# Kernel tuning notes

Hardware: AMD Instinct MI355X
Metric: run time of the kernel (lower is better)

The kernel has to match this reference:

```python
import jax, jax.numpy as jnp
import numpy as np

HALF_LOG_2PI = 0.9189385332046727  # 0.5*log(2*pi)


def _sum_layer(prod, logits):
    # prod: [B, R, KK] child log-probs; logits: [R, KK, K] unnormalized sum weights
    W = jax.nn.softmax(logits, axis=1)            # normalized mixture weights
    m = jnp.max(prod, axis=-1, keepdims=True)     # stable logsumexp via einsum
    e = jnp.exp(prod - m)                         # [B, R, KK]
    s = jnp.einsum('brc,rck->brk', e, W)          # [B, R, K]
    return jnp.log(s) + m


def setup_inputs() -> dict:
    key = jax.random.key(0)
    ks = jax.random.split(key, 12)
    B, F, K = 8192, 256, 8
    inp = {
        'x': jax.random.normal(ks[0], (B, F), dtype=jnp.float32),
        'mu': jax.random.normal(ks[1], (F, K), dtype=jnp.float32),
        'log_sigma': jax.random.uniform(ks[2], (F, K), dtype=jnp.float32),
    }
    R = F // 2
    for i in range(8):
        inp['w%d' % i] = jax.random.normal(ks[3 + i], (R, K * K, K), dtype=jnp.float32)
        R //= 2
    inp['root_w'] = jax.random.normal(ks[11], (K,), dtype=jnp.float32)
    return inp


def reference(x, mu, log_sigma, w0, w1, w2, w3, w4, w5, w6, w7, root_w):
    # Gaussian leaf log-probs: [B, F, K]
    z = (x[:, :, None] - mu) * jnp.exp(-log_sigma)
    h = -0.5 * z * z - log_sigma - HALF_LOG_2PI
    # Alternating product (pair adjacent regions) / sum (mix KK -> K) layers
    for w in (w0, w1, w2, w3, w4, w5, w6, w7):
        B, R, K = h.shape
        prod = (h[:, 0::2, :, None] + h[:, 1::2, None, :]).reshape(B, R // 2, K * K)
        h = _sum_layer(prod, w)
    # Root sum node over the K dists of the single remaining region -> [B]
    lp = h[:, 0, :] + jax.nn.log_softmax(root_w)
    return jax.scipy.special.logsumexp(lp, axis=-1)
```

## Files before the change

kernel.cpp:

```cpp
#include <hip/hip_runtime.h>
#include <math.h>

#define NTH 256

static constexpr float HLP = 0.9189385332046727f;

typedef __attribute__((ext_vector_type(2))) _Float16 half2v;
typedef __attribute__((ext_vector_type(2))) __fp16   fp16x2;

static constexpr int L3MF = 524288;
static constexpr size_t WS_NEED_B = (size_t)655360 * 4;

__device__ __forceinline__ half2v pkrtz(float a, float b) {
  return __builtin_bit_cast(half2v, __builtin_amdgcn_cvt_pkrtz(a, b));
}
__device__ __forceinline__ half2v u2h(unsigned u) {
  return __builtin_bit_cast(half2v, u);
}
__device__ __forceinline__ unsigned h2u(half2v h) {
  return __builtin_bit_cast(unsigned, h);
}
__device__ __forceinline__ float dd(half2v a, half2v b, float c) {
#if __has_builtin(__builtin_amdgcn_fdot2)
  return __builtin_amdgcn_fdot2(__builtin_bit_cast(fp16x2, a),
                                __builtin_bit_cast(fp16x2, b), c, false);
#else
  return fmaf((float)a[0], (float)b[0], fmaf((float)a[1], (float)b[1], c));
#endif
}
__device__ __forceinline__ float max8(const float* s) {
  float m = s[0];
  #pragma unroll
  for (int k = 1; k < 8; ++k) m = fmaxf(m, s[k]);
  return m;
}

__device__ __forceinline__ void leaf_ii(float xv, const float* mu8, const float* A8,
                                        const float* B8, half2v* ii, float* M) {
  float h[8];
  float m = -3.0e38f;
  #pragma unroll
  for (int k = 0; k < 8; ++k) {
    const float z = (xv - mu8[k]) * A8[k];
    h[k] = fmaf(-0.5f * z, z, B8[k]);
    m = fmaxf(m, h[k]);
  }
  #pragma unroll
  for (int k = 0; k < 8; ++k) {
    const float n = __expf(h[k] - m);
    ii[k] = pkrtz(n, n);
  }
  *M = m;
}
__device__ __forceinline__ void leaf_pk(float xv, const float* mu8, const float* A8,
                                        const float* B8, half2v* pk, float* M) {
  float h[8];
  float m = -3.0e38f;
  #pragma unroll
  for (int k = 0; k < 8; ++k) {
    const float z = (xv - mu8[k]) * A8[k];
    h[k] = fmaf(-0.5f * z, z, B8[k]);
    m = fmaxf(m, h[k]);
  }
  #pragma unroll
  for (int p = 0; p < 4; ++p) {
    const float n0 = __expf(h[2 * p] - m);
    const float n1 = __expf(h[2 * p + 1] - m);
    pk[p] = pkrtz(n0, n1);
  }
  *M = m;
}

template<int G, bool OUT_II>
__device__ __forceinline__ void combine_d2(const uint4* __restrict__ WL,
                                           const half2v (&na)[G][8],
                                           const half2v (&nb)[G][4],
                                           half2v (&oii)[G][8],
                                           half2v (&opk)[G][4],
                                           float (&M)[G]) {
  float s[G][8];
  #pragma unroll
  for (int g = 0; g < G; ++g)
    #pragma unroll
    for (int k = 0; k < 8; ++k) s[g][k] = 0.f;

  #pragma unroll
  for (int i = 0; i < 8; ++i) {
    half2v e[G][4];
    #pragma unroll
    for (int g = 0; g < G; ++g) {
      e[g][0] = na[g][i] * nb[g][0];
      e[g][1] = na[g][i] * nb[g][1];
      e[g][2] = na[g][i] * nb[g][2];
      e[g][3] = na[g][i] * nb[g][3];
    }
    #pragma unroll
    for (int k = 0; k < 8; ++k) {
      const uint4 w = WL[i * 8 + k];
      #pragma unroll
      for (int g = 0; g < G; ++g) {
        float acc = s[g][k];
        acc = dd(e[g][0], u2h(w.x), acc);
        acc = dd(e[g][1], u2h(w.y), acc);
        acc = dd(e[g][2], u2h(w.z), acc);
        acc = dd(e[g][3], u2h(w.w), acc);
        s[g][k] = acc;
      }
    }
  }
  #pragma unroll
  for (int g = 0; g < G; ++g) {
    const float smax = max8(s[g]);
    const float inv = 1.0f / smax;
    if constexpr (OUT_II) {
      #pragma unroll
      for (int p = 0; p < 8; ++p) {
        const float n = s[g][p] * inv;
        oii[g][p] = pkrtz(n, n);
      }
    } else {
      #pragma unroll
      for (int p = 0; p < 4; ++p)
        opk[g][p] = pkrtz(s[g][2 * p] * inv, s[g][2 * p + 1] * inv);
    }
    M[g] += __logf(smax);
  }
}

__device__ __forceinline__ void prep_col_std(const float* stage, unsigned* wdwL,
                                             int r, int k) {
  float v[64];
  float m = -3.0e38f;
  #pragma unroll
  for (int c = 0; c < 64; ++c) { v[c] = stage[r * 512 + c * 8 + k]; m = fmaxf(m, v[c]); }
  float t = 0.f;
  #pragma unroll
  for (int c = 0; c < 64; ++c) { v[c] = __expf(v[c] - m); t += v[c]; }
  const float inv = 1.0f / t;
  #pragma unroll
  for (int i = 0; i < 8; ++i)
    #pragma unroll
    for (int jp = 0; jp < 4; ++jp)
      wdwL[r * 256 + (i * 8 + k) * 4 + jp] =
          h2u(pkrtz(v[i * 8 + 2 * jp] * inv, v[i * 8 + 2 * jp + 1] * inv));
}

__device__ __forceinline__ void mk_ii(uint4 p, half2v* ii) {
  const half2v a0 = u2h(p.x), a1 = u2h(p.y), a2 = u2h(p.z), a3 = u2h(p.w);
  ii[0] = __builtin_shufflevector(a0, a0, 0, 0);
  ii[1] = __builtin_shufflevector(a0, a0, 1, 1);
  ii[2] = __builtin_shufflevector(a1, a1, 0, 0);
  ii[3] = __builtin_shufflevector(a1, a1, 1, 1);
  ii[4] = __builtin_shufflevector(a2, a2, 0, 0);
  ii[5] = __builtin_shufflevector(a2, a2, 1, 1);
  ii[6] = __builtin_shufflevector(a3, a3, 0, 0);
  ii[7] = __builtin_shufflevector(a3, a3, 1, 1);
}

template<bool OUT_II>
__device__ __forceinline__ void subtree_g2(
    const uint4* __restrict__ wA, const uint4* __restrict__ wB,
    const uint4* __restrict__ wT,
    const float* m0, const float* A0, const float* B0,
    float4 xa, float4 xb,
    half2v (&oii)[2][8], half2v (&opk)[2][4], float (&Mout)[2]) {
  half2v ii[2][8], pk[2][4];
  half2v aii[2][8], bpk[2][4];
  half2v dii[2][8], dpk[2][4];
  float Ma, Mb;

  leaf_ii(xa.x, m0,      A0,      B0,      ii[0], &Ma);
  leaf_pk(xa.y, m0 + 8,  A0 + 8,  B0 + 8,  pk[0], &Mb);
  float MA[2];
  MA[0] = Ma + Mb;
  leaf_ii(xb.x, m0,      A0,      B0,      ii[1], &Ma);
  leaf_pk(xb.y, m0 + 8,  A0 + 8,  B0 + 8,  pk[1], &Mb);
  MA[1] = Ma + Mb;
  combine_d2<2, true>(wA, ii, pk, aii, dpk, MA);

  leaf_ii(xa.z, m0 + 16, A0 + 16, B0 + 16, ii[0], &Ma);
  leaf_pk(xa.w, m0 + 24, A0 + 24, B0 + 24, pk[0], &Mb);
  float MB[2];
  MB[0] = Ma + Mb;
  leaf_ii(xb.z, m0 + 16, A0 + 16, B0 + 16, ii[1], &Ma);
  leaf_pk(xb.w, m0 + 24, A0 + 24, B0 + 24, pk[1], &Mb);
  MB[1] = Ma + Mb;
  combine_d2<2, false>(wB, ii, pk, dii, bpk, MB);

  float M[2] = {MA[0] + MB[0], MA[1] + MB[1]};
  combine_d2<2, OUT_II>(wT, aii, bpk, oii, opk, M);
  Mout[0] = M[0];
  Mout[1] = M[1];
}

__global__ __launch_bounds__(NTH, 2) void spn_f(
    const float* __restrict__ x,
    const float* __restrict__ mu,
    const float* __restrict__ ls,
    const float* __restrict__ w0, const float* __restrict__ w1,
    const float* __restrict__ w2, const float* __restrict__ w3,
    float* __restrict__ ws)
{
  __shared__ float stage[7680];
  __shared__ uint4 wsh4[960];
  __shared__ float lsh[384];
  const int tid = threadIdx.x;
  const int r3 = blockIdx.x >> 5;
  const int chunk = blockIdx.x & 31;

  #pragma unroll
  for (int i = 0; i < 30; ++i) {
    const int idx = tid + 256 * i;
    const int reg = idx >> 9, off = idx & 511;
    const float* src;
    if (reg < 8)       src = w0 + (8 * r3 + reg) * 512;
    else if (reg < 12) src = w1 + (4 * r3 + (reg - 8)) * 512;
    else if (reg < 14) src = w2 + (2 * r3 + (reg - 12)) * 512;
    else               src = w3 + r3 * 512;
    stage[idx] = src[off];
  }
  if (tid < 128) {
    const int base = r3 * 128;
    const float l = ls[base + tid];
    lsh[tid]       = mu[base + tid];
    lsh[128 + tid] = __expf(-l);
    lsh[256 + tid] = -l - HLP;
  }
  __syncthreads();

  if (tid < 120) prep_col_std(stage, reinterpret_cast<unsigned*>(wsh4), tid >> 3, tid & 7);
  __syncthreads();

  uint4* exN = reinterpret_cast<uint4*>(stage);
  float* exM = stage + 2048;

  const int h = tid >> 7;
  const int u = tid & 127;
  const int b0 = chunk * 256 + u;
  {
    const float* xa = x + (size_t)b0 * 256 + 16 * r3 + 8 * h;
    const float* xb = x + (size_t)(b0 + 128) * 256 + 16 * r3 + 8 * h;
    const float4 xa0 = *reinterpret_cast<const float4*>(xa);
    const float4 xa1 = *reinterpret_cast<const float4*>(xa + 4);
    const float4 xb0 = *reinterpret_cast<const float4*>(xb);
    const float4 xb1 = *reinterpret_cast<const float4*>(xb + 4);

    const float* m0 = lsh + h * 64;
    const float* A0 = lsh + 128 + h * 64;
    const float* B0 = lsh + 256 + h * 64;
    const uint4* wL0 = wsh4 + (4 * h) * 64;
    const uint4* wL1 = wsh4 + (8 + 2 * h) * 64;
    const uint4* wL2 = wsh4 + (12 + h) * 64;

    half2v q0ii[2][8], q1pk[2][4];
    half2v dii[2][8], dpk[2][4];
    float Mq0[2], Mq1[2];

    subtree_g2<true >(wL0,        wL0 + 64,  wL1,      m0,      A0,      B0,
                      xa0, xb0, q0ii, dpk, Mq0);
    subtree_g2<false>(wL0 + 128,  wL0 + 192, wL1 + 64, m0 + 32, A0 + 32, B0 + 32,
                      xa1, xb1, dii, q1pk, Mq1);

    float M[2] = {Mq0[0] + Mq1[0], Mq0[1] + Mq1[1]};
    half2v n[2][4];
    combine_d2<2, false>(wL2, q0ii, q1pk, dii, n, M);

    exN[h * 256 + u]       = uint4{h2u(n[0][0]), h2u(n[0][1]), h2u(n[0][2]), h2u(n[0][3])};
    exN[h * 256 + u + 128] = uint4{h2u(n[1][0]), h2u(n[1][1]), h2u(n[1][2]), h2u(n[1][3])};
    exM[h * 256 + u]       = M[0];
    exM[h * 256 + u + 128] = M[1];
  }
  __syncthreads();

  if (tid < 128) {
    const uint4 p0a = exN[tid], p0b = exN[tid + 128];
    const uint4 p1a = exN[256 + tid], p1b = exN[256 + tid + 128];
    float M[2];
    M[0] = exM[tid]       + exM[256 + tid];
    M[1] = exM[tid + 128] + exM[256 + tid + 128];

    half2v ii[2][8], pk[2][4];
    half2v dii[2][8];
    mk_ii(p0a, ii[0]);
    mk_ii(p0b, ii[1]);
    pk[0][0] = u2h(p1a.x); pk[0][1] = u2h(p1a.y); pk[0][2] = u2h(p1a.z); pk[0][3] = u2h(p1a.w);
    pk[1][0] = u2h(p1b.x); pk[1][1] = u2h(p1b.y); pk[1][2] = u2h(p1b.z); pk[1][3] = u2h(p1b.w);

    half2v n[2][4];
    combine_d2<2, false>(wsh4 + 14 * 64, ii, pk, dii, n, M);

    const int b = chunk * 256 + tid;
    uint4* outn = reinterpret_cast<uint4*>(ws);
    outn[r3 * 8192 + b]       = uint4{h2u(n[0][0]), h2u(n[0][1]), h2u(n[0][2]), h2u(n[0][3])};
    outn[r3 * 8192 + b + 128] = uint4{h2u(n[1][0]), h2u(n[1][1]), h2u(n[1][2]), h2u(n[1][3])};
    ws[L3MF + r3 * 8192 + b]       = M[0];
    ws[L3MF + r3 * 8192 + b + 128] = M[1];
  }
}

__device__ __forceinline__ float macTd(const uint4* __restrict__ Wr, int myk,
                                       const float* na, const half2v* nbpk) {
  float s = 0.f;
  #pragma unroll
  for (int i = 0; i < 8; ++i) {
    const uint4 w = Wr[myk * 8 + ((i ^ myk) & 7)];
    float T = dd(nbpk[0], u2h(w.x), 0.f);
    T = dd(nbpk[1], u2h(w.y), T);
    T = dd(nbpk[2], u2h(w.z), T);
    T = dd(nbpk[3], u2h(w.w), T);
    s = fmaf(na[i], T, s);
  }
  return s;
}

__global__ __launch_bounds__(NTH) void spn_c(
    const float* __restrict__ w4, const float* __restrict__ w5,
    const float* __restrict__ w6, const float* __restrict__ w7,
    const float* __restrict__ root_w,
    float* __restrict__ ws,
    float* __restrict__ out)
{
  __shared__ float stage[7680];
  __shared__ uint4 wsh4[960];
  __shared__ float ssh[8];
  const int tid = threadIdx.x;

  #pragma unroll
  for (int i = 0; i < 30; ++i) {
    const int idx = tid + 256 * i;
    const int reg = idx >> 9, off = idx & 511;
    const float* src;
    if (reg < 8)       src = w4 + reg * 512;
    else if (reg < 12) src = w5 + (reg - 8) * 512;
    else if (reg < 14) src = w6 + (reg - 12) * 512;
    else               src = w7;
    stage[idx] = src[off];
  }
  if (tid == 255) {
    float m = -3.0e38f;
    for (int k = 0; k < 8; ++k) m = fmaxf(m, root_w[k]);
    float e[8]; float t = 0.f;
    for (int k = 0; k < 8; ++k) { e[k] = __expf(root_w[k] - m); t += e[k]; }
    const float inv = 1.0f / t;
    for (int k = 0; k < 8; ++k) ssh[k] = e[k] * inv;
  }
  __syncthreads();

  if (tid < 120) {
    const int reg = tid >> 3, k = tid & 7;
    float v[64];
    float m = -3.0e38f;
    #pragma unroll
    for (int c = 0; c < 64; ++c) { v[c] = stage[reg * 512 + c * 8 + k]; m = fmaxf(m, v[c]); }
    float t = 0.f;
    #pragma unroll
    for (int c = 0; c < 64; ++c) { v[c] = __expf(v[c] - m); t += v[c]; }
    const float inv = 1.0f / t;
    unsigned* wdwL = reinterpret_cast<unsigned*>(wsh4);
    #pragma unroll
    for (int i = 0; i < 8; ++i)
      #pragma unroll
      for (int jp = 0; jp < 4; ++jp)
        wdwL[reg * 256 + k * 32 + (((i ^ k) & 7) << 2) + jp] =
            h2u(pkrtz(v[i * 8 + 2 * jp] * inv, v[i * 8 + 2 * jp + 1] * inv));
  }
  __syncthreads();

  const int lane = tid & 63, wid = tid >> 6;
  const int myk = lane & 7, bsub = lane >> 3, gbase = lane & 56;
  const int b = blockIdx.x * 32 + wid * 8 + bsub;

  const uint4* n4 = reinterpret_cast<const uint4*>(ws);

  float n4v[8], M4[8];
  #pragma unroll
  for (int r = 0; r < 8; ++r) {
    const uint4 pa = n4[(2 * r + 0) * 8192 + b];
    const uint4 pb = n4[(2 * r + 1) * 8192 + b];
    const float Ma = ws[L3MF + (2 * r + 0) * 8192 + b];
    const float Mb = ws[L3MF + (2 * r + 1) * 8192 + b];
    float na[8];
    const half2v a0 = u2h(pa.x), a1 = u2h(pa.y), a2 = u2h(pa.z), a3 = u2h(pa.w);
    na[0] = (float)a0[0]; na[1] = (float)a0[1];
    na[2] = (float)a1[0]; na[3] = (float)a1[1];
    na[4] = (float)a2[0]; na[5] = (float)a2[1];
    na[6] = (float)a3[0]; na[7] = (float)a3[1];
    half2v nbpk[4] = {u2h(pb.x), u2h(pb.y), u2h(pb.z), u2h(pb.w)};
    float s = macTd(wsh4 + r * 64, myk, na, nbpk);
    float m = s;
    m = fmaxf(m, __shfl_xor(m, 1)); m = fmaxf(m, __shfl_xor(m, 2)); m = fmaxf(m, __shfl_xor(m, 4));
    n4v[r] = s / m;
    M4[r] = Ma + Mb + __logf(m);
  }

  float n5v[4], M5[4];
  #pragma unroll
  for (int r = 0; r < 4; ++r) {
    float na[8]; half2v nbpk[4];
    #pragma unroll
    for (int i = 0; i < 8; ++i) na[i] = __shfl(n4v[2 * r], gbase + i, 64);
    #pragma unroll
    for (int p = 0; p < 4; ++p)
      nbpk[p] = pkrtz(__shfl(n4v[2 * r + 1], gbase + 2 * p, 64),
                      __shfl(n4v[2 * r + 1], gbase + 2 * p + 1, 64));
    float s = macTd(wsh4 + (8 + r) * 64, myk, na, nbpk);
    float m = s;
    m = fmaxf(m, __shfl_xor(m, 1)); m = fmaxf(m, __shfl_xor(m, 2)); m = fmaxf(m, __shfl_xor(m, 4));
    n5v[r] = s / m;
    M5[r] = M4[2 * r] + M4[2 * r + 1] + __logf(m);
  }

  float n6v[2], M6[2];
  #pragma unroll
  for (int r = 0; r < 2; ++r) {
    float na[8]; half2v nbpk[4];
    #pragma unroll
    for (int i = 0; i < 8; ++i) na[i] = __shfl(n5v[2 * r], gbase + i, 64);
    #pragma unroll
    for (int p = 0; p < 4; ++p)
      nbpk[p] = pkrtz(__shfl(n5v[2 * r + 1], gbase + 2 * p, 64),
                      __shfl(n5v[2 * r + 1], gbase + 2 * p + 1, 64));
    float s = macTd(wsh4 + (12 + r) * 64, myk, na, nbpk);
    float m = s;
    m = fmaxf(m, __shfl_xor(m, 1)); m = fmaxf(m, __shfl_xor(m, 2)); m = fmaxf(m, __shfl_xor(m, 4));
    n6v[r] = s / m;
    M6[r] = M5[2 * r] + M5[2 * r + 1] + __logf(m);
  }

  {
    float na[8]; half2v nbpk[4];
    #pragma unroll
    for (int i = 0; i < 8; ++i) na[i] = __shfl(n6v[0], gbase + i, 64);
    #pragma unroll
    for (int p = 0; p < 4; ++p)
      nbpk[p] = pkrtz(__shfl(n6v[1], gbase + 2 * p, 64),
                      __shfl(n6v[1], gbase + 2 * p + 1, 64));
    float s = macTd(wsh4 + 14 * 64, myk, na, nbpk);
    float m = s;
    m = fmaxf(m, __shfl_xor(m, 1)); m = fmaxf(m, __shfl_xor(m, 2)); m = fmaxf(m, __shfl_xor(m, 4));
    const float n7 = s / m;
    const float M7 = M6[0] + M6[1] + __logf(m);
    float prod = n7 * ssh[myk];
    prod += __shfl_xor(prod, 1); prod += __shfl_xor(prod, 2); prod += __shfl_xor(prod, 4);
    if (myk == 0) out[b] = M7 + __logf(prod);
  }
}

static constexpr int NW   = 130560;
static constexpr int AOFF = NW;
static constexpr int BOFF = NW + 2048;
static constexpr int ROFF = NW + 4096;

__device__ __forceinline__ void leaf_eval(float xv, const float* mu8, const float* A8,
                                          const float* B8, float* n, float* M) {
  float h[8];
  float m = -3.0e38f;
  #pragma unroll
  for (int k = 0; k < 8; ++k) {
    const float z = (xv - mu8[k]) * A8[k];
    h[k] = fmaf(-0.5f * z, z, B8[k]);
    m = fmaxf(m, h[k]);
  }
  #pragma unroll
  for (int k = 0; k < 8; ++k) n[k] = __expf(h[k] - m);
  *M = m;
}

__global__ __launch_bounds__(256) void spn_prep(
    const float* __restrict__ ls,
    const float* __restrict__ w0, const float* __restrict__ w1,
    const float* __restrict__ w2, const float* __restrict__ w3,
    const float* __restrict__ w4, const float* __restrict__ w5,
    const float* __restrict__ w6, const float* __restrict__ w7,
    const float* __restrict__ root_w,
    float* __restrict__ ws)
{
  const int job = blockIdx.x * blockDim.x + threadIdx.x;
  if (job < 2040) {
    const float* wl[8] = {w0, w1, w2, w3, w4, w5, w6, w7};
    int j = job, l = 0, base = 0, R = 128;
    while (j >= R * 8) { j -= R * 8; base += R * 512; R >>= 1; ++l; }
    const int r = j >> 3, k = j & 7;
    const float* src = wl[l] + r * 512 + k;
    float v[64];
    float m = -3.0e38f;
    #pragma unroll
    for (int c = 0; c < 64; ++c) { v[c] = src[c * 8]; m = fmaxf(m, v[c]); }
    float ssum = 0.f;
    #pragma unroll
    for (int c = 0; c < 64; ++c) { v[c] = __expf(v[c] - m); ssum += v[c]; }
    const float inv = 1.0f / ssum;
    float* dst = ws + base + r * 512 + k;
    #pragma unroll
    for (int c = 0; c < 64; ++c) dst[c * 8] = v[c] * inv;
  } else if (job < 2040 + 2048) {
    const int i = job - 2040;
    const float l = ls[i];
    ws[AOFF + i] = __expf(-l);
    ws[BOFF + i] = -l - HLP;
  } else if (job == 2040 + 2048) {
    float m = -3.0e38f;
    for (int k = 0; k < 8; ++k) m = fmaxf(m, root_w[k]);
    float e[8]; float ssum = 0.f;
    for (int k = 0; k < 8; ++k) { e[k] = __expf(root_w[k] - m); ssum += e[k]; }
    const float inv = 1.0f / ssum;
    for (int k = 0; k < 8; ++k) ws[ROFF + k] = e[k] * inv;
  }
}

__device__ __forceinline__ void mac64(const float* __restrict__ Wr,
                                      const float* na, const float* nb,
                                      float* s) {
  #pragma unroll
  for (int k = 0; k < 8; ++k) s[k] = 0.f;
  #pragma unroll
  for (int i = 0; i < 8; ++i) {
    const float ai = na[i];
    #pragma unroll
    for (int j = 0; j < 8; ++j) {
      const float e = ai * nb[j];
      const float4 wA = *reinterpret_cast<const float4*>(Wr + (i * 8 + j) * 8);
      const float4 wB = *reinterpret_cast<const float4*>(Wr + (i * 8 + j) * 8 + 4);
      s[0] = fmaf(e, wA.x, s[0]); s[1] = fmaf(e, wA.y, s[1]);
      s[2] = fmaf(e, wA.z, s[2]); s[3] = fmaf(e, wA.w, s[3]);
      s[4] = fmaf(e, wB.x, s[4]); s[5] = fmaf(e, wB.y, s[5]);
      s[6] = fmaf(e, wB.z, s[6]); s[7] = fmaf(e, wB.w, s[7]);
    }
  }
}

#define TB 8
static constexpr int PLA = 128 * 9 + 5;
static constexpr int PLB = 64 * 9 + 5;
static constexpr int NAO = 0;
static constexpr int NBO = TB * PLA;
static constexpr int MAO = NBO + TB * PLB;
static constexpr int MBO = MAO + TB * 128;
static constexpr int SMEM_F = MBO + TB * 64;

__global__ __launch_bounds__(NTH, 2) void spn_main_fb(
    const float* __restrict__ x,
    const float* __restrict__ mu,
    const float* __restrict__ ws,
    float* __restrict__ out)
{
  const float* leafA = ws + AOFF;
  const float* leafB = ws + BOFF;
  const float* srw   = ws + ROFF;

  __shared__ float smem[SMEM_F];

  const int tid = threadIdx.x;
  const int bB = blockIdx.x * TB;

  {
    const float* W0 = ws;
    for (int it = tid; it < TB * 128; it += NTH) {
      const int bb = it & (TB - 1), r = it >> 3;
      float na[8], nb[8], Ma, Mb;
      const int f0 = 2 * r;
      const float xv0 = x[(bB + bb) * 256 + f0];
      const float xv1 = x[(bB + bb) * 256 + f0 + 1];
      leaf_eval(xv0, mu + f0 * 8, leafA + f0 * 8, leafB + f0 * 8, na, &Ma);
      leaf_eval(xv1, mu + f0 * 8 + 8, leafA + f0 * 8 + 8, leafB + f0 * 8 + 8, nb, &Mb);
      float s[8];
      mac64(W0 + r * 512, na, nb, s);
      const float smax = max8(s);
      const float inv = 1.0f / smax;
      const int ob = NAO + bb * PLA + r * 9;
      #pragma unroll
      for (int k = 0; k < 8; ++k) smem[ob + k] = s[k] * inv;
      smem[MAO + bb * 128 + r] = Ma + Mb + __logf(smax);
    }
  }
  __syncthreads();

  int pinO = NAO, poutO = NBO;
  int MinO = MAO, MoutO = MBO;
  int PLIN = PLA, PLOUT = PLB;
  int Rin = 128;
  const float* Wl = ws + 128 * 512;
  for (int l = 1; l < 7; ++l) {
    const int Rout = Rin >> 1;
    for (int it = tid; it < TB * Rout; it += NTH) {
      const int bb = it & (TB - 1), r = it >> 3;
      float na[8], nb[8];
      const int ia = pinO + bb * PLIN + (2 * r) * 9;
      #pragma unroll
      for (int i = 0; i < 8; ++i) { na[i] = smem[ia + i]; nb[i] = smem[ia + 9 + i]; }
      float s[8];
      mac64(Wl + r * 512, na, nb, s);
      const float smax = max8(s);
      const float inv = 1.0f / smax;
      const int ob = poutO + bb * PLOUT + r * 9;
      #pragma unroll
      for (int k = 0; k < 8; ++k) smem[ob + k] = s[k] * inv;
      smem[MoutO + bb * Rout + r] =
          smem[MinO + bb * Rin + 2 * r] + smem[MinO + bb * Rin + 2 * r + 1] + __logf(smax);
    }
    __syncthreads();
    int t;
    t = pinO; pinO = poutO; poutO = t;
    t = MinO; MinO = MoutO; MoutO = t;
    t = PLIN; PLIN = PLOUT; PLOUT = t;
    Rin = Rout;
    Wl += Rout * 512;
  }

  for (int it = tid; it < TB; it += NTH) {
    const int bb = it;
    float na[8], nb[8];
    const int ia = pinO + bb * PLIN;
    #pragma unroll
    for (int i = 0; i < 8; ++i) { na[i] = smem[ia + i]; nb[i] = smem[ia + 9 + i]; }
    float s[8];
    mac64(Wl, na, nb, s);
    float acc = 0.f;
    #pragma unroll
    for (int k = 0; k < 8; ++k) acc = fmaf(s[k], srw[k], acc);
    out[bB + bb] = smem[MinO + bb * 2] + smem[MinO + bb * 2 + 1] + __logf(acc);
  }
}

extern "C" void kernel_launch(void* const* d_in, const int* in_sizes, int n_in,
                              void* d_out, int out_size, void* d_ws, size_t ws_size,
                              hipStream_t stream) {
  (void)in_sizes; (void)n_in; (void)out_size;
  const float* x      = (const float*)d_in[0];
  const float* mu     = (const float*)d_in[1];
  const float* ls     = (const float*)d_in[2];
  const float* w0     = (const float*)d_in[3];
  const float* w1     = (const float*)d_in[4];
  const float* w2     = (const float*)d_in[5];
  const float* w3     = (const float*)d_in[6];
  const float* w4     = (const float*)d_in[7];
  const float* w5     = (const float*)d_in[8];
  const float* w6     = (const float*)d_in[9];
  const float* w7     = (const float*)d_in[10];
  const float* root_w = (const float*)d_in[11];
  float* ws  = (float*)d_ws;
  float* out = (float*)d_out;

  if (ws_size >= WS_NEED_B) {
    spn_f<<<512, NTH, 0, stream>>>(x, mu, ls, w0, w1, w2, w3, ws);
    spn_c<<<256, NTH, 0, stream>>>(w4, w5, w6, w7, root_w, ws, out);
  } else {
    spn_prep<<<16, 256, 0, stream>>>(ls, w0, w1, w2, w3, w4, w5, w6, w7, root_w, ws);
    spn_main_fb<<<8192 / TB, NTH, 0, stream>>>(x, mu, ws, out);
  }
}
```

Before: 47.81 us.

## Move weight softmax prep into a separate prep kernel, read weights from global

Adds a 256-block prep kernel that softmax-normalizes every sum-layer weight table once, packs it to fp16 pairs in the workspace, and also precomputes the leaf constants and root weights. The main leaf and top kernels no longer stage and normalize weights in shared memory per block. Instead they read the packed weights directly from global memory, which removes the redundant per-block prep that 512 and 256 blocks each repeated. In exchange it adds a third kernel launch, and the hot loops now fetch weights from global memory through the cache rather than from LDS.

```diff
diff --git a/kernel.cpp b/kernel.cpp
--- a/kernel.cpp
+++ b/kernel.cpp
@@ -8,8 +8,13 @@
 typedef __attribute__((ext_vector_type(2))) _Float16 half2v;
 typedef __attribute__((ext_vector_type(2))) __fp16   fp16x2;
 
-static constexpr int L3MF = 524288;
-static constexpr size_t WS_NEED_B = (size_t)655360 * 4;
+static constexpr int WTTd = 61440;
+static constexpr int AOF2 = 65280;
+static constexpr int BOF2 = 67328;
+static constexpr int ROF2 = 69376;
+static constexpr int L3NF = 69632;
+static constexpr int L3MF = 593920;
+static constexpr size_t WS_NEED_B = (size_t)724992 * 4;
 
 __device__ __forceinline__ half2v pkrtz(float a, float b) {
   return __builtin_bit_cast(half2v, __builtin_amdgcn_cvt_pkrtz(a, b));
@@ -125,24 +130,6 @@
     }
     M[g] += __logf(smax);
   }
-}
-
-__device__ __forceinline__ void prep_col_std(const float* stage, unsigned* wdwL,
-                                             int r, int k) {
-  float v[64];
-  float m = -3.0e38f;
-  #pragma unroll
-  for (int c = 0; c < 64; ++c) { v[c] = stage[r * 512 + c * 8 + k]; m = fmaxf(m, v[c]); }
-  float t = 0.f;
-  #pragma unroll
-  for (int c = 0; c < 64; ++c) { v[c] = __expf(v[c] - m); t += v[c]; }
-  const float inv = 1.0f / t;
-  #pragma unroll
-  for (int i = 0; i < 8; ++i)
-    #pragma unroll
-    for (int jp = 0; jp < 4; ++jp)
-      wdwL[r * 256 + (i * 8 + k) * 4 + jp] =
-          h2u(pkrtz(v[i * 8 + 2 * jp] * inv, v[i * 8 + 2 * jp + 1] * inv));
 }
 
 __device__ __forceinline__ void mk_ii(uint4 p, half2v* ii) {
@@ -155,6 +142,86 @@
   ii[5] = __builtin_shufflevector(a2, a2, 1, 1);
   ii[6] = __builtin_shufflevector(a3, a3, 0, 0);
   ii[7] = __builtin_shufflevector(a3, a3, 1, 1);
+}
+
+__global__ __launch_bounds__(256) void spn_prep5(
+    const float* __restrict__ ls,
+    const float* __restrict__ w0, const float* __restrict__ w1,
+    const float* __restrict__ w2, const float* __restrict__ w3,
+    const float* __restrict__ w4, const float* __restrict__ w5,
+    const float* __restrict__ w6, const float* __restrict__ w7,
+    const float* __restrict__ root_w,
+    float* __restrict__ ws)
+{
+  const int blk = blockIdx.x;
+  const int tid = threadIdx.x;
+  unsigned* wdw = reinterpret_cast<unsigned*>(ws);
+
+  if (blk == 255) {
+    #pragma unroll
+    for (int i = 0; i < 8; ++i) {
+      const int idx = tid + i * 256;
+      const float l = ls[idx];
+      ws[AOF2 + idx] = __expf(-l);
+      ws[BOF2 + idx] = -l - HLP;
+    }
+    if (tid == 0) {
+      float m = -3.0e38f;
+      for (int k = 0; k < 8; ++k) m = fmaxf(m, root_w[k]);
+      float e[8]; float t = 0.f;
+      for (int k = 0; k < 8; ++k) { e[k] = __expf(root_w[k] - m); t += e[k]; }
+      const float inv = 1.0f / t;
+      for (int k = 0; k < 8; ++k) ws[ROF2 + k] = e[k] * inv;
+    }
+    return;
+  }
+
+  __shared__ float lsw[512];
+  const float* src;
+  bool transposed = false;
+  int reg = 0;
+  if (blk < 128)       src = w0 + blk * 512;
+  else if (blk < 192)  src = w1 + (blk - 128) * 512;
+  else if (blk < 224)  src = w2 + (blk - 192) * 512;
+  else if (blk < 240)  src = w3 + (blk - 224) * 512;
+  else {
+    transposed = true;
+    reg = blk - 240;
+    if (reg < 8)       src = w4 + reg * 512;
+    else if (reg < 12) src = w5 + (reg - 8) * 512;
+    else if (reg < 14) src = w6 + (reg - 12) * 512;
+    else               src = w7;
+  }
+  lsw[tid]       = src[tid];
+  lsw[tid + 256] = src[tid + 256];
+  __syncthreads();
+
+  if (tid < 8) {
+    const int k = tid;
+    float v[64];
+    float m = -3.0e38f;
+    #pragma unroll
+    for (int c = 0; c < 64; ++c) { v[c] = lsw[c * 8 + k]; m = fmaxf(m, v[c]); }
+    float t = 0.f;
+    #pragma unroll
+    for (int c = 0; c < 64; ++c) { v[c] = __expf(v[c] - m); t += v[c]; }
+    const float inv = 1.0f / t;
+    if (!transposed) {
+      #pragma unroll
+      for (int i = 0; i < 8; ++i)
+        #pragma unroll
+        for (int jp = 0; jp < 4; ++jp)
+          wdw[blk * 256 + (i * 8 + k) * 4 + jp] =
+              h2u(pkrtz(v[i * 8 + 2 * jp] * inv, v[i * 8 + 2 * jp + 1] * inv));
+    } else {
+      #pragma unroll
+      for (int i = 0; i < 8; ++i)
+        #pragma unroll
+        for (int jp = 0; jp < 4; ++jp)
+          wdw[WTTd + reg * 256 + k * 32 + (((i ^ k) & 7) << 2) + jp] =
+              h2u(pkrtz(v[i * 8 + 2 * jp] * inv, v[i * 8 + 2 * jp + 1] * inv));
+    }
+  }
 }
 
 template<bool OUT_II>
@@ -193,46 +260,26 @@
   Mout[1] = M[1];
 }
 
-__global__ __launch_bounds__(NTH, 2) void spn_f(
+__global__ __launch_bounds__(NTH, 2) void spn_h(
     const float* __restrict__ x,
     const float* __restrict__ mu,
-    const float* __restrict__ ls,
-    const float* __restrict__ w0, const float* __restrict__ w1,
-    const float* __restrict__ w2, const float* __restrict__ w3,
     float* __restrict__ ws)
 {
-  __shared__ float stage[7680];
-  __shared__ uint4 wsh4[960];
+  __shared__ uint4 exN[512];
+  __shared__ float exM[512];
   __shared__ float lsh[384];
   const int tid = threadIdx.x;
   const int r3 = blockIdx.x >> 5;
   const int chunk = blockIdx.x & 31;
-
-  #pragma unroll
-  for (int i = 0; i < 30; ++i) {
-    const int idx = tid + 256 * i;
-    const int reg = idx >> 9, off = idx & 511;
-    const float* src;
-    if (reg < 8)       src = w0 + (8 * r3 + reg) * 512;
-    else if (reg < 12) src = w1 + (4 * r3 + (reg - 8)) * 512;
-    else if (reg < 14) src = w2 + (2 * r3 + (reg - 12)) * 512;
-    else               src = w3 + r3 * 512;
-    stage[idx] = src[off];
-  }
+  const uint4* __restrict__ wg = reinterpret_cast<const uint4*>(ws);
+
   if (tid < 128) {
     const int base = r3 * 128;
-    const float l = ls[base + tid];
     lsh[tid]       = mu[base + tid];
-    lsh[128 + tid] = __expf(-l);
-    lsh[256 + tid] = -l - HLP;
+    lsh[128 + tid] = ws[AOF2 + base + tid];
+    lsh[256 + tid] = ws[BOF2 + base + tid];
   }
   __syncthreads();
-
-  if (tid < 120) prep_col_std(stage, reinterpret_cast<unsigned*>(wsh4), tid >> 3, tid & 7);
-  __syncthreads();
-
-  uint4* exN = reinterpret_cast<uint4*>(stage);
-  float* exM = stage + 2048;
 
   const int h = tid >> 7;
   const int u = tid & 127;
@@ -248,9 +295,9 @@
     const float* m0 = lsh + h * 64;
     const float* A0 = lsh + 128 + h * 64;
     const float* B0 = lsh + 256 + h * 64;
-    const uint4* wL0 = wsh4 + (4 * h) * 64;
-    const uint4* wL1 = wsh4 + (8 + 2 * h) * 64;
-    const uint4* wL2 = wsh4 + (12 + h) * 64;
+    const uint4* wL0 = wg + (size_t)(8 * r3 + 4 * h) * 64;
+    const uint4* wL1 = wg + (size_t)(128 + 4 * r3 + 2 * h) * 64;
+    const uint4* wL2 = wg + (size_t)(192 + 2 * r3 + h) * 64;
 
     half2v q0ii[2][8], q1pk[2][4];
     half2v dii[2][8], dpk[2][4];
@@ -287,10 +334,10 @@
     pk[1][0] = u2h(p1b.x); pk[1][1] = u2h(p1b.y); pk[1][2] = u2h(p1b.z); pk[1][3] = u2h(p1b.w);
 
     half2v n[2][4];
-    combine_d2<2, false>(wsh4 + 14 * 64, ii, pk, dii, n, M);
+    combine_d2<2, false>(wg + (size_t)(224 + r3) * 64, ii, pk, dii, n, M);
 
     const int b = chunk * 256 + tid;
-    uint4* outn = reinterpret_cast<uint4*>(ws);
+    uint4* outn = reinterpret_cast<uint4*>(ws + L3NF);
     outn[r3 * 8192 + b]       = uint4{h2u(n[0][0]), h2u(n[0][1]), h2u(n[0][2]), h2u(n[0][3])};
     outn[r3 * 8192 + b + 128] = uint4{h2u(n[1][0]), h2u(n[1][1]), h2u(n[1][2]), h2u(n[1][3])};
     ws[L3MF + r3 * 8192 + b]       = M[0];
@@ -313,64 +360,22 @@
   return s;
 }
 
-__global__ __launch_bounds__(NTH) void spn_c(
-    const float* __restrict__ w4, const float* __restrict__ w5,
-    const float* __restrict__ w6, const float* __restrict__ w7,
-    const float* __restrict__ root_w,
+__global__ __launch_bounds__(NTH) void spn_c2g(
     float* __restrict__ ws,
     float* __restrict__ out)
 {
-  __shared__ float stage[7680];
-  __shared__ uint4 wsh4[960];
   __shared__ float ssh[8];
   const int tid = threadIdx.x;
-
-  #pragma unroll
-  for (int i = 0; i < 30; ++i) {
-    const int idx = tid + 256 * i;
-    const int reg = idx >> 9, off = idx & 511;
-    const float* src;
-    if (reg < 8)       src = w4 + reg * 512;
-    else if (reg < 12) src = w5 + (reg - 8) * 512;
-    else if (reg < 14) src = w6 + (reg - 12) * 512;
-    else               src = w7;
-    stage[idx] = src[off];
-  }
-  if (tid == 255) {
-    float m = -3.0e38f;
-    for (int k = 0; k < 8; ++k) m = fmaxf(m, root_w[k]);
-    float e[8]; float t = 0.f;
-    for (int k = 0; k < 8; ++k) { e[k] = __expf(root_w[k] - m); t += e[k]; }
-    const float inv = 1.0f / t;
-    for (int k = 0; k < 8; ++k) ssh[k] = e[k] * inv;
-  }
-  __syncthreads();
-
-  if (tid < 120) {
-    const int reg = tid >> 3, k = tid & 7;
-    float v[64];
-    float m = -3.0e38f;
-    #pragma unroll
-    for (int c = 0; c < 64; ++c) { v[c] = stage[reg * 512 + c * 8 + k]; m = fmaxf(m, v[c]); }
-    float t = 0.f;
-    #pragma unroll
-    for (int c = 0; c < 64; ++c) { v[c] = __expf(v[c] - m); t += v[c]; }
-    const float inv = 1.0f / t;
-    unsigned* wdwL = reinterpret_cast<unsigned*>(wsh4);
-    #pragma unroll
-    for (int i = 0; i < 8; ++i)
-      #pragma unroll
-      for (int jp = 0; jp < 4; ++jp)
-        wdwL[reg * 256 + k * 32 + (((i ^ k) & 7) << 2) + jp] =
-            h2u(pkrtz(v[i * 8 + 2 * jp] * inv, v[i * 8 + 2 * jp + 1] * inv));
-  }
+  const uint4* __restrict__ wt = reinterpret_cast<const uint4*>(ws) + WTTd / 4;
+
+  if (tid < 8) ssh[tid] = ws[ROF2 + tid];
   __syncthreads();
 
   const int lane = tid & 63, wid = tid >> 6;
   const int myk = lane & 7, bsub = lane >> 3, gbase = lane & 56;
   const int b = blockIdx.x * 32 + wid * 8 + bsub;
 
-  const uint4* n4 = reinterpret_cast<const uint4*>(ws);
+  const uint4* n4 = reinterpret_cast<const uint4*>(ws + L3NF);
 
   float n4v[8], M4[8];
   #pragma unroll
@@ -386,7 +391,7 @@
     na[4] = (float)a2[0]; na[5] = (float)a2[1];
     na[6] = (float)a3[0]; na[7] = (float)a3[1];
     half2v nbpk[4] = {u2h(pb.x), u2h(pb.y), u2h(pb.z), u2h(pb.w)};
-    float s = macTd(wsh4 + r * 64, myk, na, nbpk);
+    float s = macTd(wt + r * 64, myk, na, nbpk);
     float m = s;
     m = fmaxf(m, __shfl_xor(m, 1)); m = fmaxf(m, __shfl_xor(m, 2)); m = fmaxf(m, __shfl_xor(m, 4));
     n4v[r] = s / m;
@@ -403,7 +408,7 @@
     for (int p = 0; p < 4; ++p)
       nbpk[p] = pkrtz(__shfl(n4v[2 * r + 1], gbase + 2 * p, 64),
                       __shfl(n4v[2 * r + 1], gbase + 2 * p + 1, 64));
-    float s = macTd(wsh4 + (8 + r) * 64, myk, na, nbpk);
+    float s = macTd(wt + (8 + r) * 64, myk, na, nbpk);
     float m = s;
     m = fmaxf(m, __shfl_xor(m, 1)); m = fmaxf(m, __shfl_xor(m, 2)); m = fmaxf(m, __shfl_xor(m, 4));
     n5v[r] = s / m;
@@ -420,7 +425,7 @@
     for (int p = 0; p < 4; ++p)
       nbpk[p] = pkrtz(__shfl(n5v[2 * r + 1], gbase + 2 * p, 64),
                       __shfl(n5v[2 * r + 1], gbase + 2 * p + 1, 64));
-    float s = macTd(wsh4 + (12 + r) * 64, myk, na, nbpk);
+    float s = macTd(wt + (12 + r) * 64, myk, na, nbpk);
     float m = s;
     m = fmaxf(m, __shfl_xor(m, 1)); m = fmaxf(m, __shfl_xor(m, 2)); m = fmaxf(m, __shfl_xor(m, 4));
     n6v[r] = s / m;
@@ -435,7 +440,7 @@
     for (int p = 0; p < 4; ++p)
       nbpk[p] = pkrtz(__shfl(n6v[1], gbase + 2 * p, 64),
                       __shfl(n6v[1], gbase + 2 * p + 1, 64));
-    float s = macTd(wsh4 + 14 * 64, myk, na, nbpk);
+    float s = macTd(wt + 14 * 64, myk, na, nbpk);
     float m = s;
     m = fmaxf(m, __shfl_xor(m, 1)); m = fmaxf(m, __shfl_xor(m, 2)); m = fmaxf(m, __shfl_xor(m, 4));
     const float n7 = s / m;
@@ -642,8 +647,9 @@
   float* out = (float*)d_out;
 
   if (ws_size >= WS_NEED_B) {
-    spn_f<<<512, NTH, 0, stream>>>(x, mu, ls, w0, w1, w2, w3, ws);
-    spn_c<<<256, NTH, 0, stream>>>(w4, w5, w6, w7, root_w, ws, out);
+    spn_prep5<<<256, 256, 0, stream>>>(ls, w0, w1, w2, w3, w4, w5, w6, w7, root_w, ws);
+    spn_h<<<512, NTH, 0, stream>>>(x, mu, ws);
+    spn_c2g<<<256, NTH, 0, stream>>>(ws, out);
   } else {
     spn_prep<<<16, 256, 0, stream>>>(ls, w0, w1, w2, w3, w4, w5, w6, w7, root_w, ws);
     spn_main_fb<<<8192 / TB, NTH, 0, stream>>>(x, mu, ws, out);
```

Measured after the change: 63.52 us. 32.9% more time.
